# Optimization experiments

Hardware: AMD Instinct MI355X
Metric: run time of the kernel (lower is better)

The kernel has to match this reference:

```python
import jax, jax.numpy as jnp
import numpy as np

N = 16384      # bs(2048) * n_agents(8)
D_IN = 256     # input_shape
H = 256        # rnn_hidden_dim
E = 256        # hypernet_embed
A = 32         # n_actions


def setup_inputs() -> dict:
    key = jax.random.key(0)
    ks = jax.random.split(key, 18)
    s = 0.05
    f32 = jnp.float32
    return {
        "x": jax.random.normal(ks[0], (N, D_IN), f32),
        "h": jax.random.normal(ks[1], (N, H), f32) * 0.1,
        "fc1_w": jax.random.normal(ks[2], (D_IN, H), f32) * s,
        "fc1_b": jnp.zeros((H,), f32),
        "gru_w_ih": jax.random.normal(ks[3], (H, 3 * H), f32) * s,
        "gru_b_ih": jnp.zeros((3 * H,), f32),
        "gru_w_hh": jax.random.normal(ks[4], (H, 3 * H), f32) * s,
        "gru_b_hh": jnp.zeros((3 * H,), f32),
        "hg_w1": jax.random.normal(ks[5], (H, E), f32) * s,
        "hg_b1": jnp.zeros((E,), f32),
        "hg_w2": jax.random.normal(ks[6], (E, E), f32) * s,
        "hg_b2": jnp.zeros((E,), f32),
        "hb_w": jax.random.normal(ks[7], (E, A), f32) * s,
        "hb_b": jnp.zeros((A,), f32),
        "hw_w": jax.random.normal(ks[8], (E, H * A), f32) * s,
        "hw_b": jnp.zeros((H * A,), f32),
    }


def _gru_cell(x, h, w_ih, b_ih, w_hh, b_hh):
    # torch.nn.GRUCell semantics (gate order: r, z, n)
    gi = x @ w_ih + b_ih            # [N, 3H]
    gh = h @ w_hh + b_hh            # [N, 3H]
    i_r, i_z, i_n = jnp.split(gi, 3, axis=-1)
    h_r, h_z, h_n = jnp.split(gh, 3, axis=-1)
    r = jax.nn.sigmoid(i_r + h_r)
    z = jax.nn.sigmoid(i_z + h_z)
    n = jnp.tanh(i_n + r * h_n)
    return (1.0 - z) * n + z * h


def reference(x, h, fc1_w, fc1_b, gru_w_ih, gru_b_ih, gru_w_hh, gru_b_hh,
              hg_w1, hg_b1, hg_w2, hg_b2, hb_w, hb_b, hw_w, hw_b):
    x1 = jax.nn.relu(x @ fc1_w + fc1_b)                       # [N, H]
    hn = _gru_cell(x1, h, gru_w_ih, gru_b_ih, gru_w_hh, gru_b_hh)  # [N, H]
    # hypernet latent
    g = jnp.tanh(jax.nn.relu(hn @ hg_w1 + hg_b1) @ hg_w2 + hg_b2)  # [N, E]
    b_dyn = g @ hb_w + hb_b                                    # [N, A]
    w_dyn = (g @ hw_w + hw_b).reshape(hn.shape[0], H, A)       # [N, H, A]
    q = jnp.einsum('nh,nha->na', hn, w_dyn) + b_dyn            # [N, A]
    return q
```

## Files before the change

### kernel.cpp

```cpp
#include <hip/hip_runtime.h>


typedef _Float16 half8 __attribute__((ext_vector_type(8)));
typedef float f32x4 __attribute__((ext_vector_type(4)));

#define MFMA16(a, b, c) __builtin_amdgcn_mfma_f32_16x16x32_f16((a), (b), (c), 0, 0, 0)

constexpr int NROWS = 16384;

__device__ __forceinline__ float sigmoidf_(float x) { return 1.0f / (1.0f + __expf(-x)); }

__device__ __forceinline__ void glds16(const _Float16* g, _Float16* l) {
    __builtin_amdgcn_global_load_lds((const __attribute__((address_space(1))) void*)g,
                                     (__attribute__((address_space(3))) void*)l, 16, 0, 0);
}

__global__ void cvt_kernel(const float* __restrict__ x, const float* __restrict__ h,
                           _Float16* __restrict__ x16, _Float16* __restrict__ xh) {
    int b = blockIdx.x;
    if (b < 4096) {
        int i = (b * 256 + threadIdx.x) * 4;
        float4 v = *reinterpret_cast<const float4*>(x + i);
        x16[i + 0] = (_Float16)v.x; x16[i + 1] = (_Float16)v.y;
        x16[i + 2] = (_Float16)v.z; x16[i + 3] = (_Float16)v.w;
    } else {
        int i = ((b - 4096) * 256 + threadIdx.x) * 4;
        float4 v = *reinterpret_cast<const float4*>(h + i);
        int n = i >> 8, j = i & 255;
        _Float16* o = xh + n * 512 + 256 + j;
        o[0] = (_Float16)v.x; o[1] = (_Float16)v.y;
        o[2] = (_Float16)v.z; o[3] = (_Float16)v.w;
    }
}

__global__ void wtrans_kernel(const float* __restrict__ s0, const float* __restrict__ s1,
                              const float* __restrict__ s2, const float* __restrict__ s3,
                              const float* __restrict__ s4, _Float16* __restrict__ d0,
                              _Float16* __restrict__ d1, _Float16* __restrict__ d2,
                              _Float16* __restrict__ d3, _Float16* __restrict__ d4) {
    __shared__ float tile[32][33];
    int b = blockIdx.x;
    const float* src; _Float16* dst; int C, idx;
    if (b < 64)       { src = s0; dst = d0; C = 256;  idx = b; }
    else if (b < 128) { src = s1; dst = d1; C = 256;  idx = b - 64; }
    else if (b < 192) { src = s2; dst = d2; C = 256;  idx = b - 128; }
    else if (b < 200) { src = s3; dst = d3; C = 32;   idx = b - 192; }
    else              { src = s4; dst = d4; C = 8192; idx = b - 200; }
    int kb = (idx & 7) * 32, cb = (idx >> 3) * 32;
    int tx = threadIdx.x, ty = threadIdx.y;
#pragma unroll
    for (int i = ty; i < 32; i += 8) tile[i][tx] = src[(kb + i) * C + cb + tx];
    __syncthreads();
#pragma unroll
    for (int i = ty; i < 32; i += 8) {
        int c = cb + i, k = kb + tx;
        dst[c * 256 + (k ^ ((c & 7) << 3))] = (_Float16)tile[tx][i];
    }
}

__global__ void wgru_prep_kernel(const float* __restrict__ gwih, const float* __restrict__ gwhh,
                                 _Float16* __restrict__ wgru) {
    int t = blockIdx.x * 256 + threadIdx.x;
    int row = t >> 6, k0 = (t & 63) << 3;
    int gate = (row >> 4) & 3, c = (row >> 6) * 16 + (row & 15);
    half8 v;
#pragma unroll
    for (int e = 0; e < 8; e++) {
        int k = k0 + e;
        float f;
        if (gate == 0) f = (k < 256) ? gwih[k * 768 + c] : gwhh[(k - 256) * 768 + c];
        else if (gate == 1) f = (k < 256) ? gwih[k * 768 + 256 + c] : gwhh[(k - 256) * 768 + 256 + c];
        else if (gate == 2) f = (k < 256) ? gwih[k * 768 + 512 + c] : 0.0f;
        else f = (k < 256) ? 0.0f : gwhh[(k - 256) * 768 + 512 + c];
        v[e] = (_Float16)f;
    }
    *reinterpret_cast<half8*>(wgru + row * 512 + (k0 ^ ((row & 7) << 3))) = v;
}

template <int ACT>
__global__ __launch_bounds__(256, 2) void gemm_lds_kernel(
    const _Float16* __restrict__ Am, const _Float16* __restrict__ Wt,
    const float* __restrict__ bias, _Float16* __restrict__ out16, int ONC) {
    __shared__ _Float16 Bs[64 * 256];
    const int tid = threadIdx.x, wave = tid >> 6, lane = tid & 63;
    const int r = lane & 15, kg = lane >> 4;
    const int row0 = blockIdx.x * 256 + wave * 64;
    const int col0 = blockIdx.y * 64;
    const _Float16* src = Wt + col0 * 256;
#pragma unroll
    for (int it = 0; it < 8; ++it)
        glds16(src + it * 2048 + tid * 8, Bs + it * 2048 + tid * 8);
    asm volatile("s_waitcnt vmcnt(0)");
    __syncthreads();

    f32x4 z = {0.f, 0.f, 0.f, 0.f};
    f32x4 acc[4][4];
#pragma unroll
    for (int t = 0; t < 4; t++)
#pragma unroll
        for (int j = 0; j < 4; j++) acc[t][j] = z;
    const int swz = (r & 7) << 4;
#pragma unroll
    for (int kb = 0; kb < 8; kb++) {
        half8 a[4], bm[4];
#pragma unroll
        for (int t = 0; t < 4; t++)
            a[t] = *reinterpret_cast<const half8*>(Am + (row0 + t * 16 + r) * 256 + kb * 32 + kg * 8);
#pragma unroll
        for (int j = 0; j < 4; j++)
            bm[j] = *reinterpret_cast<const half8*>(
                (const char*)Bs + (j * 16 + r) * 512 + ((kb * 64 + kg * 16) ^ swz));
#pragma unroll
        for (int t = 0; t < 4; t++)
#pragma unroll
            for (int j = 0; j < 4; j++) acc[t][j] = MFMA16(a[t], bm[j], acc[t][j]);
    }
#pragma unroll
    for (int j = 0; j < 4; j++) {
        int cc = col0 + j * 16 + r;
        float bv = bias[cc];
#pragma unroll
        for (int t = 0; t < 4; t++)
#pragma unroll
            for (int i = 0; i < 4; i++) {
                int rr = row0 + t * 16 + kg * 4 + i;
                float v = acc[t][j][i] + bv;
                if (ACT == 1) v = fmaxf(v, 0.0f);
                if (ACT == 2) v = tanhf(v);
                out16[rr * ONC + cc] = (_Float16)v;
            }
    }
}

__global__ __launch_bounds__(256, 2) void gru_kernel(
    const _Float16* __restrict__ xh, const float* __restrict__ hf,
    const _Float16* __restrict__ wgru, const float* __restrict__ bih,
    const float* __restrict__ bhh, _Float16* __restrict__ hn16) {
    __shared__ _Float16 Bs[64 * 512];
    const int tid = threadIdx.x, wave = tid >> 6, lane = tid & 63;
    const int r = lane & 15, kg = lane >> 4;
    const int row0 = blockIdx.x * 256 + wave * 64;
    const int c0 = blockIdx.y * 16;
    const _Float16* src = wgru + (size_t)blockIdx.y * 64 * 512;
#pragma unroll
    for (int it = 0; it < 16; ++it)
        glds16(src + it * 2048 + tid * 8, Bs + it * 2048 + tid * 8);
    asm volatile("s_waitcnt vmcnt(0)");
    __syncthreads();

    f32x4 z = {0.f, 0.f, 0.f, 0.f};
    f32x4 acc[4][4];
#pragma unroll
    for (int t = 0; t < 4; t++)
#pragma unroll
        for (int j = 0; j < 4; j++) acc[t][j] = z;
    const int swz = (r & 7) << 4;
#pragma unroll
    for (int kb = 0; kb < 16; kb++) {
        half8 a[4], bm[4];
#pragma unroll
        for (int t = 0; t < 4; t++)
            a[t] = *reinterpret_cast<const half8*>(xh + (row0 + t * 16 + r) * 512 + kb * 32 + kg * 8);
#pragma unroll
        for (int j = 0; j < 4; j++)
            bm[j] = *reinterpret_cast<const half8*>(
                (const char*)Bs + (j * 16 + r) * 1024 + ((kb * 64 + kg * 16) ^ swz));
#pragma unroll
        for (int t = 0; t < 4; t++)
#pragma unroll
            for (int j = 0; j < 4; j++) acc[t][j] = MFMA16(a[t], bm[j], acc[t][j]);
    }
    const int cc = c0 + r;
    float brz = bih[cc] + bhh[cc];
    float bzz = bih[256 + cc] + bhh[256 + cc];
    float bin = bih[512 + cc], bhn = bhh[512 + cc];
#pragma unroll
    for (int t = 0; t < 4; t++)
#pragma unroll
        for (int i = 0; i < 4; i++) {
            int rr = row0 + t * 16 + kg * 4 + i;
            float rg = sigmoidf_(acc[t][0][i] + brz);
            float zg = sigmoidf_(acc[t][1][i] + bzz);
            float nn = tanhf(acc[t][2][i] + bin + rg * (acc[t][3][i] + bhn));
            float v = (1.0f - zg) * nn + zg * hf[rr * 256 + cc];
            hn16[rr * 256 + cc] = (_Float16)v;
        }
}

__global__ void hnt_kernel(const _Float16* __restrict__ hn16, float* __restrict__ hnT) {
    __shared__ float tile[32][33];
    int r0 = blockIdx.x * 32, c0 = blockIdx.y * 32;
    int tx = threadIdx.x, ty = threadIdx.y;
#pragma unroll
    for (int i = ty; i < 32; i += 8) tile[i][tx] = (float)hn16[(r0 + i) * 256 + c0 + tx];
    __syncthreads();
#pragma unroll
    for (int i = ty; i < 32; i += 8) hnT[(size_t)(c0 + i) * NROWS + r0 + tx] = tile[tx][i];
}

__global__ __launch_bounds__(256, 2) void final_kernel(
    const _Float16* __restrict__ g16, const _Float16* __restrict__ hwt,
    const float* __restrict__ hwb, const _Float16* __restrict__ hbt,
    const float* __restrict__ hbb, const float* __restrict__ hnT,
    float* __restrict__ q) {
    __shared__ _Float16 Bs[2][16384];
    __shared__ float hwbs[1024];
    const int tid = threadIdx.x, wave = tid >> 6, lane = tid & 63;
    const int r = lane & 15, kg = lane >> 4;
    const int row0 = blockIdx.x * 256 + wave * 64;
    const int hbase = blockIdx.y * 32;
    const int swz = (r & 7) << 4;

    half8 ga[4][8];
#pragma unroll
    for (int t = 0; t < 4; t++)
#pragma unroll
        for (int kb = 0; kb < 8; kb++)
            ga[t][kb] = *reinterpret_cast<const half8*>(g16 + (row0 + t * 16 + r) * 256 + kb * 32 + kg * 8);
#pragma unroll
    for (int t = 0; t < 4; t++)
#pragma unroll
        for (int kb = 0; kb < 8; kb++)
            asm volatile("" : "+v"(ga[t][kb]));

    {
        const _Float16* src = hwt + (size_t)hbase * 8192;
#pragma unroll
        for (int it = 0; it < 8; ++it)
            glds16(src + it * 2048 + tid * 8, &Bs[0][0] + it * 2048 + tid * 8);
        *reinterpret_cast<float4*>(&hwbs[tid * 4]) =
            *reinterpret_cast<const float4*>(hwb + hbase * 32 + tid * 4);
    }

    f32x4 qa[4][2];
    if (blockIdx.y == 0) {
        float b0v = hbb[r], b1v = hbb[16 + r];
#pragma unroll
        for (int t = 0; t < 4; t++) {
            qa[t][0] = {b0v, b0v, b0v, b0v};
            qa[t][1] = {b1v, b1v, b1v, b1v};
        }
#pragma unroll
        for (int kb = 0; kb < 8; kb++) {
            half8 hb0 = *reinterpret_cast<const half8*>(
                (const char*)hbt + r * 512 + ((kb * 64 + kg * 16) ^ swz));
            half8 hb1 = *reinterpret_cast<const half8*>(
                (const char*)hbt + (16 + r) * 512 + ((kb * 64 + kg * 16) ^ swz));
#pragma unroll
            for (int t = 0; t < 4; t++) {
                qa[t][0] = MFMA16(ga[t][kb], hb0, qa[t][0]);
                qa[t][1] = MFMA16(ga[t][kb], hb1, qa[t][1]);
            }
        }
    } else {
        f32x4 z = {0.f, 0.f, 0.f, 0.f};
#pragma unroll
        for (int t = 0; t < 4; t++) { qa[t][0] = z; qa[t][1] = z; }
    }

    asm volatile("s_waitcnt vmcnt(0)");
    __syncthreads();

    for (int c = 0; c < 16; ++c) {
        const int b = c & 1;
        if (c < 15) {
            const _Float16* src = hwt + (size_t)(hbase + (c + 1) * 2) * 8192;
            _Float16* dst = &Bs[b ^ 1][0];
#pragma unroll
            for (int it = 0; it < 8; ++it)
                glds16(src + it * 2048 + tid * 8, dst + it * 2048 + tid * 8);
        }
#pragma unroll
        for (int hh = 0; hh < 2; ++hh) {
            const int hloc = c * 2 + hh;
            const int h = hbase + hloc;
            const char* bp = (const char*)&Bs[b][hh * 8192];
            float wb0 = hwbs[hloc * 32 + r], wb1 = hwbs[hloc * 32 + 16 + r];
            f32x4 w[4][2];
#pragma unroll
            for (int t = 0; t < 4; t++) {
                w[t][0] = {wb0, wb0, wb0, wb0};
                w[t][1] = {wb1, wb1, wb1, wb1};
            }
#pragma unroll
            for (int kb = 0; kb < 8; kb++) {
                const int c0b = (kb * 64 + kg * 16) ^ swz;
                half8 b0 = *reinterpret_cast<const half8*>(bp + r * 512 + c0b);
                half8 b1 = *reinterpret_cast<const half8*>(bp + (16 + r) * 512 + c0b);
#pragma unroll
                for (int t = 0; t < 4; t++) {
                    w[t][0] = MFMA16(ga[t][kb], b0, w[t][0]);
                    w[t][1] = MFMA16(ga[t][kb], b1, w[t][1]);
                }
            }
#pragma unroll
            for (int t = 0; t < 4; t++) {
                f32x4 hv = *reinterpret_cast<const f32x4*>(hnT + (size_t)h * NROWS + row0 + t * 16 + kg * 4);
#pragma unroll
                for (int i = 0; i < 4; i++) {
                    qa[t][0][i] += hv[i] * w[t][0][i];
                    qa[t][1][i] += hv[i] * w[t][1][i];
                }
            }
        }
        asm volatile("s_waitcnt vmcnt(0)");
        __syncthreads();
    }

#pragma unroll
    for (int t = 0; t < 4; t++)
#pragma unroll
        for (int i = 0; i < 4; i++) {
            int rr = row0 + t * 16 + kg * 4 + i;
            atomicAdd(&q[rr * 32 + r], qa[t][0][i]);
            atomicAdd(&q[rr * 32 + 16 + r], qa[t][1][i]);
        }
}

extern "C" void kernel_launch(void* const* d_in, const int* in_sizes, int n_in,
                              void* d_out, int out_size, void* d_ws, size_t ws_size,
                              hipStream_t stream) {
    const float* x = (const float*)d_in[0];
    const float* h = (const float*)d_in[1];
    const float* fc1_w = (const float*)d_in[2];
    const float* fc1_b = (const float*)d_in[3];
    const float* gwih = (const float*)d_in[4];
    const float* gbih = (const float*)d_in[5];
    const float* gwhh = (const float*)d_in[6];
    const float* gbhh = (const float*)d_in[7];
    const float* hgw1 = (const float*)d_in[8];
    const float* hgb1 = (const float*)d_in[9];
    const float* hgw2 = (const float*)d_in[10];
    const float* hgb2 = (const float*)d_in[11];
    const float* hbw = (const float*)d_in[12];
    const float* hbb = (const float*)d_in[13];
    const float* hww = (const float*)d_in[14];
    const float* hwb = (const float*)d_in[15];
    float* q = (float*)d_out;

    char* p = (char*)d_ws;
    auto alloc = [&](size_t bytes) { char* r = p; p += (bytes + 255) & ~255ULL; return r; };
    _Float16* x16 = (_Float16*)alloc((size_t)NROWS * 256 * 2);
    _Float16* xh = (_Float16*)alloc((size_t)NROWS * 512 * 2);
    _Float16* w1t = (_Float16*)alloc((size_t)256 * 256 * 2);
    _Float16* wgru = (_Float16*)alloc((size_t)1024 * 512 * 2);
    _Float16* hg1t = (_Float16*)alloc((size_t)256 * 256 * 2);
    _Float16* hg2t = (_Float16*)alloc((size_t)256 * 256 * 2);
    _Float16* hbt = (_Float16*)alloc((size_t)32 * 256 * 2);
    _Float16* hwt = (_Float16*)alloc((size_t)8192 * 256 * 2);
    _Float16* hn16 = (_Float16*)alloc((size_t)NROWS * 256 * 2);
    float* hnT = (float*)alloc((size_t)256 * NROWS * 4);
    _Float16* t16 = (_Float16*)alloc((size_t)NROWS * 256 * 2);
    _Float16* g16 = (_Float16*)alloc((size_t)NROWS * 256 * 2);

    cvt_kernel<<<8192, 256, 0, stream>>>(x, h, x16, xh);
    wtrans_kernel<<<2248, dim3(32, 8), 0, stream>>>(fc1_w, hgw1, hgw2, hbw, hww,
                                                    w1t, hg1t, hg2t, hbt, hwt);
    wgru_prep_kernel<<<256, 256, 0, stream>>>(gwih, gwhh, wgru);

    hipMemsetAsync(d_out, 0, (size_t)NROWS * 32 * sizeof(float), stream);

    gemm_lds_kernel<1><<<dim3(64, 4), 256, 0, stream>>>(x16, w1t, fc1_b, xh, 512);

    gru_kernel<<<dim3(64, 16), 256, 0, stream>>>(xh, h, wgru, gbih, gbhh, hn16);
    hnt_kernel<<<dim3(512, 8), dim3(32, 8), 0, stream>>>(hn16, hnT);

    gemm_lds_kernel<1><<<dim3(64, 4), 256, 0, stream>>>(hn16, hg1t, hgb1, t16, 256);
    gemm_lds_kernel<2><<<dim3(64, 4), 256, 0, stream>>>(t16, hg2t, hgb2, g16, 256);

    final_kernel<<<dim3(64, 8), 256, 0, stream>>>(g16, hwt, hwb, hbt, hbb, hnT, q);
}
```

Measured before the change: 188.7 us.

## Triple-buffer final kernel weight stream, stage fp16 hn in LDS, tile GRU weight prep

The final kernel now streams one hypernet weight slice per iteration through a three-deep LDS ring with partial vmcnt waits instead of double-buffering two slices with full drains. Transposed hn is stored as fp16 and preloaded into LDS with async global-to-LDS copies, replacing per-iteration fp32 global loads. The grid is linearised so blocks sharing an output row tile are adjacent, and launch bounds drop to one block per SIMD. Separately, the GRU weight prep becomes a coalesced LDS tile transpose after a memset, and the LDS-wait asm gains memory clobbers. The fp16 hn values add a little rounding error, and the lower occupancy may reduce latency hiding.

```diff
diff --git a/kernel.cpp b/kernel.cpp
--- a/kernel.cpp
+++ b/kernel.cpp
@@ -10,7 +10,7 @@
 
 __device__ __forceinline__ float sigmoidf_(float x) { return 1.0f / (1.0f + __expf(-x)); }
 
-__device__ __forceinline__ void glds16(const _Float16* g, _Float16* l) {
+__device__ __forceinline__ void glds16(const void* g, void* l) {
     __builtin_amdgcn_global_load_lds((const __attribute__((address_space(1))) void*)g,
                                      (__attribute__((address_space(3))) void*)l, 16, 0, 0);
 }
@@ -60,21 +60,24 @@
 
 __global__ void wgru_prep_kernel(const float* __restrict__ gwih, const float* __restrict__ gwhh,
                                  _Float16* __restrict__ wgru) {
-    int t = blockIdx.x * 256 + threadIdx.x;
-    int row = t >> 6, k0 = (t & 63) << 3;
-    int gate = (row >> 4) & 3, c = (row >> 6) * 16 + (row & 15);
-    half8 v;
-#pragma unroll
-    for (int e = 0; e < 8; e++) {
-        int k = k0 + e;
-        float f;
-        if (gate == 0) f = (k < 256) ? gwih[k * 768 + c] : gwhh[(k - 256) * 768 + c];
-        else if (gate == 1) f = (k < 256) ? gwih[k * 768 + 256 + c] : gwhh[(k - 256) * 768 + 256 + c];
-        else if (gate == 2) f = (k < 256) ? gwih[k * 768 + 512 + c] : 0.0f;
-        else f = (k < 256) ? 0.0f : gwhh[(k - 256) * 768 + 512 + c];
-        v[e] = (_Float16)f;
-    }
-    *reinterpret_cast<half8*>(wgru + row * 512 + (k0 ^ ((row & 7) << 3))) = v;
+    __shared__ float tile[32][33];
+    int b = blockIdx.x, job = b >> 6, idx = b & 63;
+    int kb = (idx & 7) * 32, cb = (idx >> 3) * 32;
+    const float* src = (job & 1) ? gwhh : gwih;
+    int coff = (job >> 1) * 256;
+    int gate = (job < 4) ? (job >> 1) : (2 + (job & 1));
+    int koff = (job & 1) * 256;
+    int tx = threadIdx.x, ty = threadIdx.y;
+#pragma unroll
+    for (int i = ty; i < 32; i += 8) tile[i][tx] = src[(kb + i) * 768 + coff + cb + tx];
+    __syncthreads();
+#pragma unroll
+    for (int i = ty; i < 32; i += 8) {
+        int c = cb + i;
+        int row = (c >> 4) * 64 + gate * 16 + (c & 15);
+        int kk = kb + tx + koff;
+        wgru[row * 512 + (kk ^ ((row & 7) << 3))] = (_Float16)tile[tx][i];
+    }
 }
 
 template <int ACT>
@@ -90,7 +93,7 @@
 #pragma unroll
     for (int it = 0; it < 8; ++it)
         glds16(src + it * 2048 + tid * 8, Bs + it * 2048 + tid * 8);
-    asm volatile("s_waitcnt vmcnt(0)");
+    asm volatile("s_waitcnt vmcnt(0)" ::: "memory");
     __syncthreads();
 
     f32x4 z = {0.f, 0.f, 0.f, 0.f};
@@ -145,7 +148,7 @@
 #pragma unroll
     for (int it = 0; it < 16; ++it)
         glds16(src + it * 2048 + tid * 8, Bs + it * 2048 + tid * 8);
-    asm volatile("s_waitcnt vmcnt(0)");
+    asm volatile("s_waitcnt vmcnt(0)" ::: "memory");
     __syncthreads();
 
     f32x4 z = {0.f, 0.f, 0.f, 0.f};
@@ -187,7 +190,7 @@
         }
 }
 
-__global__ void hnt_kernel(const _Float16* __restrict__ hn16, float* __restrict__ hnT) {
+__global__ void hnt_kernel(const _Float16* __restrict__ hn16, _Float16* __restrict__ hnT16) {
     __shared__ float tile[32][33];
     int r0 = blockIdx.x * 32, c0 = blockIdx.y * 32;
     int tx = threadIdx.x, ty = threadIdx.y;
@@ -195,21 +198,42 @@
     for (int i = ty; i < 32; i += 8) tile[i][tx] = (float)hn16[(r0 + i) * 256 + c0 + tx];
     __syncthreads();
 #pragma unroll
-    for (int i = ty; i < 32; i += 8) hnT[(size_t)(c0 + i) * NROWS + r0 + tx] = tile[tx][i];
-}
-
-__global__ __launch_bounds__(256, 2) void final_kernel(
+    for (int i = ty; i < 32; i += 8)
+        hnT16[(size_t)(c0 + i) * NROWS + r0 + tx] = (_Float16)tile[tx][i];
+}
+
+__global__ __launch_bounds__(256, 1) void final_kernel(
     const _Float16* __restrict__ g16, const _Float16* __restrict__ hwt,
     const float* __restrict__ hwb, const _Float16* __restrict__ hbt,
-    const float* __restrict__ hbb, const float* __restrict__ hnT,
+    const float* __restrict__ hbb, const _Float16* __restrict__ hnT16,
     float* __restrict__ q) {
-    __shared__ _Float16 Bs[2][16384];
+    __shared__ _Float16 Bs[3][8192];
+    __shared__ _Float16 hvs[8192];
     __shared__ float hwbs[1024];
+    const int bid = blockIdx.x;
+    const int by = bid & 7, bx = bid >> 3;
     const int tid = threadIdx.x, wave = tid >> 6, lane = tid & 63;
     const int r = lane & 15, kg = lane >> 4;
-    const int row0 = blockIdx.x * 256 + wave * 64;
-    const int hbase = blockIdx.y * 32;
+    const int row0 = bx * 256 + wave * 64;
+    const int hbase = by * 32;
     const int swz = (r & 7) << 4;
+
+#pragma unroll
+    for (int it = 0; it < 4; ++it) {
+        int e = it * 2048 + tid * 8;
+        glds16(hnT16 + (size_t)(hbase + (e >> 8)) * NROWS + bx * 256 + (e & 255), hvs + e);
+    }
+    glds16(hwb + hbase * 32 + tid * 4, hwbs + tid * 4);
+#pragma unroll
+    for (int it = 0; it < 4; ++it) {
+        int e = it * 2048 + tid * 8;
+        glds16(hwt + (size_t)hbase * 8192 + e, &Bs[0][0] + e);
+    }
+#pragma unroll
+    for (int it = 0; it < 4; ++it) {
+        int e = it * 2048 + tid * 8;
+        glds16(hwt + (size_t)(hbase + 1) * 8192 + e, &Bs[1][0] + e);
+    }
 
     half8 ga[4][8];
 #pragma unroll
@@ -217,23 +241,9 @@
 #pragma unroll
         for (int kb = 0; kb < 8; kb++)
             ga[t][kb] = *reinterpret_cast<const half8*>(g16 + (row0 + t * 16 + r) * 256 + kb * 32 + kg * 8);
-#pragma unroll
-    for (int t = 0; t < 4; t++)
-#pragma unroll
-        for (int kb = 0; kb < 8; kb++)
-            asm volatile("" : "+v"(ga[t][kb]));
-
-    {
-        const _Float16* src = hwt + (size_t)hbase * 8192;
-#pragma unroll
-        for (int it = 0; it < 8; ++it)
-            glds16(src + it * 2048 + tid * 8, &Bs[0][0] + it * 2048 + tid * 8);
-        *reinterpret_cast<float4*>(&hwbs[tid * 4]) =
-            *reinterpret_cast<const float4*>(hwb + hbase * 32 + tid * 4);
-    }
 
     f32x4 qa[4][2];
-    if (blockIdx.y == 0) {
+    if (by == 0) {
         float b0v = hbb[r], b1v = hbb[16 + r];
 #pragma unroll
         for (int t = 0; t < 4; t++) {
@@ -242,10 +252,9 @@
         }
 #pragma unroll
         for (int kb = 0; kb < 8; kb++) {
-            half8 hb0 = *reinterpret_cast<const half8*>(
-                (const char*)hbt + r * 512 + ((kb * 64 + kg * 16) ^ swz));
-            half8 hb1 = *reinterpret_cast<const half8*>(
-                (const char*)hbt + (16 + r) * 512 + ((kb * 64 + kg * 16) ^ swz));
+            const int c0b = (kb * 64 + kg * 16) ^ swz;
+            half8 hb0 = *reinterpret_cast<const half8*>((const char*)hbt + r * 512 + c0b);
+            half8 hb1 = *reinterpret_cast<const half8*>((const char*)hbt + (16 + r) * 512 + c0b);
 #pragma unroll
             for (int t = 0; t < 4; t++) {
                 qa[t][0] = MFMA16(ga[t][kb], hb0, qa[t][0]);
@@ -258,53 +267,53 @@
         for (int t = 0; t < 4; t++) { qa[t][0] = z; qa[t][1] = z; }
     }
 
-    asm volatile("s_waitcnt vmcnt(0)");
-    __syncthreads();
-
-    for (int c = 0; c < 16; ++c) {
-        const int b = c & 1;
-        if (c < 15) {
-            const _Float16* src = hwt + (size_t)(hbase + (c + 1) * 2) * 8192;
-            _Float16* dst = &Bs[b ^ 1][0];
-#pragma unroll
-            for (int it = 0; it < 8; ++it)
-                glds16(src + it * 2048 + tid * 8, dst + it * 2048 + tid * 8);
-        }
-#pragma unroll
-        for (int hh = 0; hh < 2; ++hh) {
-            const int hloc = c * 2 + hh;
-            const int h = hbase + hloc;
-            const char* bp = (const char*)&Bs[b][hh * 8192];
-            float wb0 = hwbs[hloc * 32 + r], wb1 = hwbs[hloc * 32 + 16 + r];
-            f32x4 w[4][2];
+    int cur = 0;
+    for (int h = 0; h < 32; ++h) {
+        if (h < 30)
+            asm volatile("s_waitcnt vmcnt(4)" ::: "memory");
+        else
+            asm volatile("s_waitcnt vmcnt(0)" ::: "memory");
+        __builtin_amdgcn_s_barrier();
+        if (h < 30) {
+            int pre = cur + 2; if (pre >= 3) pre -= 3;
+            const _Float16* src = hwt + (size_t)(hbase + h + 2) * 8192;
+            _Float16* dst = &Bs[pre][0];
+#pragma unroll
+            for (int it = 0; it < 4; ++it) {
+                int e = it * 2048 + tid * 8;
+                glds16(src + e, dst + e);
+            }
+        }
+        const char* bp = (const char*)&Bs[cur][0];
+        float wb0 = hwbs[h * 32 + r], wb1 = hwbs[h * 32 + 16 + r];
+        f32x4 w[4][2];
+#pragma unroll
+        for (int t = 0; t < 4; t++) {
+            w[t][0] = {wb0, wb0, wb0, wb0};
+            w[t][1] = {wb1, wb1, wb1, wb1};
+        }
+#pragma unroll
+        for (int kb = 0; kb < 8; kb++) {
+            const int c0b = (kb * 64 + kg * 16) ^ swz;
+            half8 b0 = *reinterpret_cast<const half8*>(bp + r * 512 + c0b);
+            half8 b1 = *reinterpret_cast<const half8*>(bp + (16 + r) * 512 + c0b);
 #pragma unroll
             for (int t = 0; t < 4; t++) {
-                w[t][0] = {wb0, wb0, wb0, wb0};
-                w[t][1] = {wb1, wb1, wb1, wb1};
-            }
-#pragma unroll
-            for (int kb = 0; kb < 8; kb++) {
-                const int c0b = (kb * 64 + kg * 16) ^ swz;
-                half8 b0 = *reinterpret_cast<const half8*>(bp + r * 512 + c0b);
-                half8 b1 = *reinterpret_cast<const half8*>(bp + (16 + r) * 512 + c0b);
-#pragma unroll
-                for (int t = 0; t < 4; t++) {
-                    w[t][0] = MFMA16(ga[t][kb], b0, w[t][0]);
-                    w[t][1] = MFMA16(ga[t][kb], b1, w[t][1]);
-                }
-            }
-#pragma unroll
-            for (int t = 0; t < 4; t++) {
-                f32x4 hv = *reinterpret_cast<const f32x4*>(hnT + (size_t)h * NROWS + row0 + t * 16 + kg * 4);
-#pragma unroll
-                for (int i = 0; i < 4; i++) {
-                    qa[t][0][i] += hv[i] * w[t][0][i];
-                    qa[t][1][i] += hv[i] * w[t][1][i];
-                }
-            }
-        }
-        asm volatile("s_waitcnt vmcnt(0)");
-        __syncthreads();
+                w[t][0] = MFMA16(ga[t][kb], b0, w[t][0]);
+                w[t][1] = MFMA16(ga[t][kb], b1, w[t][1]);
+            }
+        }
+#pragma unroll
+        for (int t = 0; t < 4; t++) {
+            const _Float16* hp = hvs + h * 256 + wave * 64 + t * 16 + kg * 4;
+            f32x4 hv = {(float)hp[0], (float)hp[1], (float)hp[2], (float)hp[3]};
+#pragma unroll
+            for (int i = 0; i < 4; i++) {
+                qa[t][0][i] += hv[i] * w[t][0][i];
+                qa[t][1][i] += hv[i] * w[t][1][i];
+            }
+        }
+        cur = cur + 1; if (cur >= 3) cur -= 3;
     }
 
 #pragma unroll
@@ -349,24 +358,25 @@
     _Float16* hbt = (_Float16*)alloc((size_t)32 * 256 * 2);
     _Float16* hwt = (_Float16*)alloc((size_t)8192 * 256 * 2);
     _Float16* hn16 = (_Float16*)alloc((size_t)NROWS * 256 * 2);
-    float* hnT = (float*)alloc((size_t)256 * NROWS * 4);
+    _Float16* hnT16 = (_Float16*)alloc((size_t)256 * NROWS * 2);
     _Float16* t16 = (_Float16*)alloc((size_t)NROWS * 256 * 2);
     _Float16* g16 = (_Float16*)alloc((size_t)NROWS * 256 * 2);
 
     cvt_kernel<<<8192, 256, 0, stream>>>(x, h, x16, xh);
     wtrans_kernel<<<2248, dim3(32, 8), 0, stream>>>(fc1_w, hgw1, hgw2, hbw, hww,
                                                     w1t, hg1t, hg2t, hbt, hwt);
-    wgru_prep_kernel<<<256, 256, 0, stream>>>(gwih, gwhh, wgru);
+    hipMemsetAsync(wgru, 0, (size_t)1024 * 512 * 2, stream);
+    wgru_prep_kernel<<<384, dim3(32, 8), 0, stream>>>(gwih, gwhh, wgru);
 
     hipMemsetAsync(d_out, 0, (size_t)NROWS * 32 * sizeof(float), stream);
 
     gemm_lds_kernel<1><<<dim3(64, 4), 256, 0, stream>>>(x16, w1t, fc1_b, xh, 512);
 
     gru_kernel<<<dim3(64, 16), 256, 0, stream>>>(xh, h, wgru, gbih, gbhh, hn16);
-    hnt_kernel<<<dim3(512, 8), dim3(32, 8), 0, stream>>>(hn16, hnT);
+    hnt_kernel<<<dim3(512, 8), dim3(32, 8), 0, stream>>>(hn16, hnT16);
 
     gemm_lds_kernel<1><<<dim3(64, 4), 256, 0, stream>>>(hn16, hg1t, hgb1, t16, 256);
     gemm_lds_kernel<2><<<dim3(64, 4), 256, 0, stream>>>(t16, hg2t, hgb2, g16, 256);
 
-    final_kernel<<<dim3(64, 8), 256, 0, stream>>>(g16, hwt, hwb, hbt, hbb, hnT, q);
-}
+    final_kernel<<<512, 256, 0, stream>>>(g16, hwt, hwb, hbt, hbb, hnT16, q);
+}
```

After: 185.1 us. No clear change (-1.9%).
